# Kernel optimization log

Measured on AMD Instinct MI355X. Metric: run time of the kernel, lower is better.

The kernel has to match this reference:

```python
import jax, jax.numpy as jnp
import numpy as np

# dims
B, L, H, NH, D = 512, 200, 128, 4, 32      # batch, seq_len, hidden, heads (gnn & fcb), head dim H/NH
FT, TP, IP = 32, 64, 200                    # first_taxonomy_num, taxonomy/item nodes per graph
NHOP, NB = 2, 2                             # n_hop gnn layers, gip_block_nums
SH, FH = 512, 256                           # scb_hidden_units, fcb_hidden_units
ITEMS, TAX = 100001, 2000                   # item vocab (+pad row 0), taxonomy vocab
NT, NI = B * TP, B * IP                     # total taxonomy / item nodes in batched forest
DEG_I, DEG_T = 4, 2                         # in-degree per taxonomy node for i2t / t2t edges


def _ln(x, g, b, eps=1e-8):
    m = jnp.mean(x, -1, keepdims=True)
    v = jnp.mean((x - m) ** 2, -1, keepdims=True)
    return (x - m) / jnp.sqrt(v + eps) * g + b


def _gat(src_h, dst_h, es, ed, W, al, ar, bias):
    """DGL GATConv (eval mode): shared fc, leaky_relu(0.2) scores, segment softmax,
    identity residual (in == heads*out), bias, ReLU activation."""
    fs = (src_h @ W).reshape(-1, NH, D)                 # [Ns,NH,D]
    fd = (dst_h @ W).reshape(-1, NH, D)                 # [Nd,NH,D]
    el = jnp.sum(fs * al, -1)                           # [Ns,NH]
    er = jnp.sum(fd * ar, -1)                           # [Nd,NH]
    e = jax.nn.leaky_relu(el[es] + er[ed], 0.2)         # [E,NH]
    emax = jax.ops.segment_max(e, ed, num_segments=NT)
    a = jnp.exp(e - emax[ed])
    s = jax.ops.segment_sum(a, ed, num_segments=NT)
    alpha = a / s[ed]                                   # [E,NH]
    rst = jax.ops.segment_sum(alpha[..., None] * fs[es], ed, num_segments=NT)
    rst = rst + dst_h.reshape(-1, NH, D) + bias.reshape(NH, D)
    return jax.nn.relu(rst).reshape(-1, NH * D)


def _forward(item_embed, tax_embed, scb_ln_g, scb_ln_b, scb_w1, scb_w2, fcb_ln_g, fcb_ln_b,
             fcb_w1, fcb_w2, fcb_w3, wv, gi_w, gi_al, gi_ar, gi_b, gt_w, gt_al, gt_ar, gt_b,
             liw_g, liw_b, int_g, int_b, uni_w,
             seq, root, i2t_src, i2t_dst, t2t_src, t2t_dst, item_ids, tax_ids):
    # --- global intention: mixer-style blocks over the item sequence ---
    V = item_embed[seq]                                           # [B,L,H]
    for i in range(NB):
        nv = _ln(V, scb_ln_g[i], scb_ln_b[i])
        t = jax.nn.gelu(jnp.einsum('blh,ls->bhs', nv, scb_w1[i]), approximate=False)
        vs = nv + jnp.einsum('bhs,sl->blh', t, scb_w2[i])         # seq-mixing block
        nvs = _ln(vs, fcb_ln_g[i], fcb_ln_b[i])
        xh = nvs.reshape(B, L, NH, D)                             # fcb heads share w1/w2
        y = jax.nn.gelu(jnp.einsum('blkc,cf->blkf', xh, fcb_w1[i]), approximate=False)
        y = jnp.einsum('blkf,fc->blkc', y, fcb_w2[i]).reshape(B, L, H)
        V = nvs + y @ fcb_w3[i]
    alpha = jax.nn.softmax(V @ wv, axis=1)                        # [B,L]
    g = jnp.sum(alpha[..., None] * V, axis=1)                     # [B,H]
    # --- local intention: multi-hop hetero GAT on batched item-taxonomy forest ---
    item_h = item_embed[item_ids]                                 # [NI,H]
    tax_h = tax_embed[tax_ids]                                    # [NT,H]
    acc = jnp.zeros_like(tax_h)
    for hop in range(NHOP):
        t_i = _gat(item_h, tax_h, i2t_src, i2t_dst, gi_w[hop], gi_al[hop], gi_ar[hop], gi_b[hop])
        t_t = _gat(tax_h, tax_h, t2t_src, t2t_dst, gt_w[hop], gt_al[hop], gt_ar[hop], gt_b[hop])
        tax_h = t_i + t_t                                         # HeteroGraphConv 'sum'
        acc = acc + tax_h                                         # k_list accumulation
    total = acc / NHOP                                            # average over hops
    offs = jnp.arange(B) * TP                                     # batched-graph offsets (graph_taxonomy)
    valid = root != -1
    local = jnp.where(valid[..., None], total[jnp.clip(root, 0) + offs[:, None]], 0.0)  # [B,FT,H]
    # --- fuse global + local ---
    mul = jnp.einsum('bfh,bh->bf', local, g)                      # [B,FT]
    w = jax.nn.softmax(jnp.where(mul != 0, _ln(mul, liw_g, liw_b), -jnp.inf), axis=-1)
    intention = _ln(g + jnp.sum(w[..., None] * local, axis=1), int_g, int_b)
    return (intention @ uni_w) @ item_embed.T                     # [B, ITEMS]


def setup_inputs():
    key = jax.random.key(0)
    ks = jax.random.split(key, 32)
    nrm = lambda i, sh: jax.random.normal(ks[i], sh, jnp.float32) * 0.05
    inp = {}
    inp['seq'] = jax.random.randint(ks[0], (B, L), 0, ITEMS)
    inp['root'] = jax.random.randint(ks[1], (B, FT), 0, TP)       # all valid roots
    i2t_dst = jnp.repeat(jnp.arange(NT), DEG_I)
    inp['i2t_dst'] = i2t_dst
    inp['i2t_src'] = (i2t_dst // TP) * IP + jax.random.randint(ks[2], (NT * DEG_I,), 0, IP)
    t2t_dst = jnp.repeat(jnp.arange(NT), DEG_T)
    inp['t2t_dst'] = t2t_dst
    inp['t2t_src'] = (t2t_dst // TP) * TP + jax.random.randint(ks[3], (NT * DEG_T,), 0, TP)
    inp['item_ids'] = jax.random.randint(ks[4], (NI,), 1, ITEMS)
    inp['tax_ids'] = jax.random.randint(ks[5], (NT,), 1, TAX)
    inp['item_embed'] = nrm(6, (ITEMS, H)).at[0].set(0.0)         # padding_idx=0
    inp['tax_embed'] = nrm(7, (TAX, H)).at[0].set(0.0)
    inp['scb_ln_g'] = jnp.ones((NB, H)); inp['scb_ln_b'] = jnp.zeros((NB, H))
    inp['scb_w1'] = nrm(8, (NB, L, SH)); inp['scb_w2'] = nrm(9, (NB, SH, L))
    inp['fcb_ln_g'] = jnp.ones((NB, H)); inp['fcb_ln_b'] = jnp.zeros((NB, H))
    inp['fcb_w1'] = nrm(10, (NB, D, FH)); inp['fcb_w2'] = nrm(11, (NB, FH, D))
    inp['fcb_w3'] = nrm(12, (NB, H, H))
    inp['wv'] = nrm(13, (H,))
    inp['gi_w'] = nrm(14, (NHOP, H, H)); inp['gi_al'] = nrm(15, (NHOP, NH, D))
    inp['gi_ar'] = nrm(16, (NHOP, NH, D)); inp['gi_b'] = nrm(17, (NHOP, H))
    inp['gt_w'] = nrm(18, (NHOP, H, H)); inp['gt_al'] = nrm(19, (NHOP, NH, D))
    inp['gt_ar'] = nrm(20, (NHOP, NH, D)); inp['gt_b'] = nrm(21, (NHOP, H))
    inp['liw_g'] = jnp.ones((FT,)); inp['liw_b'] = jnp.zeros((FT,))
    inp['int_g'] = jnp.ones((H,)); inp['int_b'] = jnp.zeros((H,))
    inp['uni_w'] = nrm(22, (H, H))
    return inp


def reference(item_embed, tax_embed, scb_ln_g, scb_ln_b, scb_w1, scb_w2, fcb_ln_g, fcb_ln_b,
              fcb_w1, fcb_w2, fcb_w3, wv, gi_w, gi_al, gi_ar, gi_b, gt_w, gt_al, gt_ar, gt_b,
              liw_g, liw_b, int_g, int_b, uni_w,
              seq, root, i2t_src, i2t_dst, t2t_src, t2t_dst, item_ids, tax_ids):
    return _forward(item_embed, tax_embed, scb_ln_g, scb_ln_b, scb_w1, scb_w2, fcb_ln_g, fcb_ln_b,
                    fcb_w1, fcb_w2, fcb_w3, wv, gi_w, gi_al, gi_ar, gi_b, gt_w, gt_al, gt_ar, gt_b,
                    liw_g, liw_b, int_g, int_b, uni_w,
                    seq, root, i2t_src, i2t_dst, t2t_src, t2t_dst, item_ids, tax_ids)
```

## Files before the change

### kernel.cpp

```cpp
#include <hip/hip_runtime.h>
#include <hip/hip_bf16.h>

constexpr int TB = 512, TL = 200, TH = 128, TNH = 4, TD = 32;
constexpr int TFT = 32, TTP = 64, TIP = 200;
constexpr int TSH = 512, TFH = 256;
constexpr int TITEMS = 100001;
constexpr int TNT = TB * TTP;
constexpr int TNI = TB * TIP;
constexpr int TLP = 224;
constexpr int TIPAD = 100096;

typedef __attribute__((ext_vector_type(8))) short short8v;
typedef __attribute__((ext_vector_type(4))) float f32x4;

__device__ inline float gelu_fast(float x) {
    float u = x + 0.044715f * x * x * x;
    float e = exp2f(-2.302208f * u);
    return x / (1.0f + e);
}
__device__ inline unsigned short to_bf16u(float x) {
    __hip_bfloat16 h = __float2bfloat16(x);
    return *reinterpret_cast<unsigned short*>(&h);
}
__device__ inline float bfu_to_f(unsigned short u) {
    unsigned int x = ((unsigned int)u) << 16;
    return __uint_as_float(x);
}

__device__ inline float block_reduce_sum(float v, float* red) {
    for (int o = 32; o > 0; o >>= 1) v += __shfl_down(v, o, 64);
    int nw = blockDim.x >> 6;
    if ((threadIdx.x & 63) == 0) red[threadIdx.x >> 6] = v;
    __syncthreads();
    float r = 0.f;
    for (int w = 0; w < nw; ++w) r += red[w];
    __syncthreads();
    return r;
}

__global__ __launch_bounds__(256) void k_gather(const float* __restrict__ tab,
                                                const int* __restrict__ idx,
                                                float* __restrict__ out, int nrows) {
    int e = blockIdx.x * blockDim.x + threadIdx.x;
    if (e >= nrows * 32) return;
    int r = e >> 5, c = e & 31;
    ((float4*)out)[e] = ((const float4*)tab)[(size_t)idx[r] * 32 + c];
}

__global__ __launch_bounds__(256) void k_gather_bf(const float* __restrict__ tab,
                                                   const int* __restrict__ idx,
                                                   unsigned short* __restrict__ out, int nrows) {
    int e = blockIdx.x * blockDim.x + threadIdx.x;
    if (e >= nrows * 16) return;
    int r = e >> 4, c = e & 15;
    const float4 a = ((const float4*)tab)[(size_t)idx[r] * 32 + c * 2];
    const float4 b = ((const float4*)tab)[(size_t)idx[r] * 32 + c * 2 + 1];
    uint4 u;
    u.x = (unsigned int)to_bf16u(a.x) | ((unsigned int)to_bf16u(a.y) << 16);
    u.y = (unsigned int)to_bf16u(a.z) | ((unsigned int)to_bf16u(a.w) << 16);
    u.z = (unsigned int)to_bf16u(b.x) | ((unsigned int)to_bf16u(b.y) << 16);
    u.w = (unsigned int)to_bf16u(b.z) | ((unsigned int)to_bf16u(b.w) << 16);
    *(uint4*)(out + (size_t)e * 8) = u;
}

__global__ __launch_bounds__(256) void k_wcvt(const float* __restrict__ fw1, const float* __restrict__ fw2,
                                              const float* __restrict__ fw3, const float* __restrict__ giw,
                                              const float* __restrict__ gtw, unsigned short* __restrict__ WB) {
    int idx = blockIdx.x * 256 + threadIdx.x;
    float v;
    if (idx < 16384) {
        int nb = idx >> 13, r = idx & 8191, n = r >> 5, k = r & 31;
        v = fw1[(size_t)nb * 8192 + k * 256 + n];
    } else if (idx < 32768) {
        int t = idx - 16384;
        int nb = t >> 13, r = t & 8191, n = r >> 8, k = r & 255;
        v = fw2[(size_t)nb * 8192 + k * 32 + n];
    } else if (idx < 65536) {
        int t = idx - 32768;
        int nb = t >> 14, r = t & 16383, n = r >> 7, k = r & 127;
        v = fw3[(size_t)nb * 16384 + k * 128 + n];
    } else if (idx < 98304) {
        int t = idx - 65536;
        int hop = t >> 14, r = t & 16383, n = r >> 7, k = r & 127;
        v = giw[(size_t)hop * 16384 + k * 128 + n];
    } else {
        int t = idx - 98304;
        int hop = t >> 14, r = t & 16383, n = r >> 7, k = r & 127;
        v = gtw[(size_t)hop * 16384 + k * 128 + n];
    }
    WB[idx] = to_bf16u(v);
}

__global__ __launch_bounds__(128) void k_lnt(const float* __restrict__ V,
                                             const float* __restrict__ g, const float* __restrict__ b,
                                             float* __restrict__ NV, unsigned short* __restrict__ NVT) {
    __shared__ float tl[64][129];
    __shared__ float mrow[64], irow[64];
    int bb = blockIdx.y, l0 = blockIdx.x * 64, tid = threadIdx.x;
    for (int i = tid; i < 2048; i += 128) {
        int r = i >> 5, c = i & 31;
        int l = l0 + r;
        float4 v = {0.f, 0.f, 0.f, 0.f};
        if (l < TL) v = *(const float4*)(V + ((size_t)bb * TL + l) * TH + c * 4);
        tl[r][c * 4 + 0] = v.x; tl[r][c * 4 + 1] = v.y;
        tl[r][c * 4 + 2] = v.z; tl[r][c * 4 + 3] = v.w;
    }
    __syncthreads();
    {
        int row = tid >> 1, half = tid & 1;
        float s = 0.f, sq = 0.f;
        for (int k = 0; k < 64; ++k) {
            float v = tl[row][half * 64 + k];
            s += v; sq += v * v;
        }
        s += __shfl_xor(s, 1);
        sq += __shfl_xor(sq, 1);
        if (half == 0) {
            float mean = s * (1.f / 128.f);
            mrow[row] = mean;
            irow[row] = rsqrtf(sq * (1.f / 128.f) - mean * mean + 1e-8f);
        }
    }
    __syncthreads();
    for (int i = tid; i < 2048; i += 128) {
        int r = i >> 5, c = i & 31;
        int l = l0 + r;
        float4 o = {0.f, 0.f, 0.f, 0.f};
        if (l < TL) {
            float4 v = *(float4*)&tl[r][c * 4];
            float m = mrow[r], inv = irow[r];
            const float4 gg = ((const float4*)g)[c];
            const float4 bv = ((const float4*)b)[c];
            o.x = (v.x - m) * inv * gg.x + bv.x;
            o.y = (v.y - m) * inv * gg.y + bv.y;
            o.z = (v.z - m) * inv * gg.z + bv.z;
            o.w = (v.w - m) * inv * gg.w + bv.w;
            *(float4*)(NV + ((size_t)bb * TL + l) * TH + c * 4) = o;
        }
        *(float4*)&tl[r][c * 4] = o;
    }
    __syncthreads();
    int h = tid;
    int ng = (l0 + 64 > TLP) ? (TLP - l0) / 8 : 8;
    for (int lg = 0; lg < ng; ++lg) {
        uint4 u;
        unsigned int p[4];
#pragma unroll
        for (int q = 0; q < 4; ++q) {
            unsigned short ua = to_bf16u(tl[lg * 8 + q * 2 + 0][h]);
            unsigned short ub = to_bf16u(tl[lg * 8 + q * 2 + 1][h]);
            p[q] = (unsigned int)ua | ((unsigned int)ub << 16);
        }
        u.x = p[0]; u.y = p[1]; u.z = p[2]; u.w = p[3];
        *(uint4*)(NVT + ((size_t)bb * TH + h) * TLP + l0 + lg * 8) = u;
    }
}

__global__ __launch_bounds__(256) void k_wscb(const float* __restrict__ w1, const float* __restrict__ w2,
                                              unsigned short* __restrict__ W1T,
                                              unsigned short* __restrict__ W2T) {
    int bx = blockIdx.x;
    if (bx < TSH) {
        int s = bx, l = threadIdx.x;
        if (l < TLP) W1T[(size_t)s * TLP + l] = to_bf16u(l < TL ? w1[(size_t)l * TSH + s] : 0.f);
    } else {
        int l = bx - TSH;
        for (int it = 0; it < 2; ++it) {
            int s = it * 256 + threadIdx.x;
            W2T[(size_t)l * TSH + s] = to_bf16u(l < TL ? w2[(size_t)s * TL + l] : 0.f);
        }
    }
}

__global__ __launch_bounds__(256) void k_mm1(const unsigned short* __restrict__ NVT,
                                             const unsigned short* __restrict__ W1T,
                                             unsigned short* __restrict__ T, int bh) {
    __shared__ unsigned short As[128][40];
    __shared__ unsigned short Bs[128][40];
    int tid = threadIdx.x;
    int b_local = blockIdx.y, b = bh * 256 + b_local;
    int s0 = blockIdx.x * 128;
    int lane = tid & 63, wid = tid >> 6;
    int mw = wid >> 1, nw = wid & 1;
    f32x4 acc[4][4];
#pragma unroll
    for (int i = 0; i < 4; ++i)
#pragma unroll
        for (int j = 0; j < 4; ++j) acc[i][j] = (f32x4){0.f, 0.f, 0.f, 0.f};
    const unsigned short* Abase = NVT + (size_t)b * TH * TLP;
    const unsigned short* Bbase = W1T + (size_t)s0 * TLP;
    for (int kc = 0; kc < 7; ++kc) {
        __syncthreads();
        for (int i = tid; i < 512; i += 256) {
            int r = i >> 2, q = i & 3;
            *(uint4*)&As[r][q * 8] = *(const uint4*)(Abase + (size_t)r * TLP + kc * 32 + q * 8);
            *(uint4*)&Bs[r][q * 8] = *(const uint4*)(Bbase + (size_t)r * TLP + kc * 32 + q * 8);
        }
        __syncthreads();
        int ko = (lane >> 4) * 8;
        short8v af[4], bfr[4];
#pragma unroll
        for (int t = 0; t < 4; ++t) {
            af[t] = *(const short8v*)&As[mw * 64 + t * 16 + (lane & 15)][ko];
            bfr[t] = *(const short8v*)&Bs[nw * 64 + t * 16 + (lane & 15)][ko];
        }
#pragma unroll
        for (int i = 0; i < 4; ++i)
#pragma unroll
            for (int j = 0; j < 4; ++j)
                acc[i][j] = __builtin_amdgcn_mfma_f32_16x16x32_bf16(af[i], bfr[j], acc[i][j], 0, 0, 0);
    }
    int rbase = (lane >> 4) * 4, col = lane & 15;
#pragma unroll
    for (int i = 0; i < 4; ++i)
#pragma unroll
        for (int j = 0; j < 4; ++j) {
            int h0 = mw * 64 + i * 16 + rbase;
            int s = s0 + nw * 64 + j * 16 + col;
#pragma unroll
            for (int r = 0; r < 4; ++r)
                T[((size_t)b_local * TH + h0 + r) * TSH + s] = to_bf16u(gelu_fast(acc[i][j][r]));
        }
}

__global__ __launch_bounds__(256) void k_mm2l(const unsigned short* __restrict__ T,
                                              const unsigned short* __restrict__ W2T,
                                              float* __restrict__ NV,
                                              const float* __restrict__ lg, const float* __restrict__ lb,
                                              int bh) {
    __shared__ unsigned short As[128][40];
    __shared__ unsigned short Bs[64][40];
    __shared__ float vsl[64][132];
    __shared__ float mrow[64], irow[64];
    int tid = threadIdx.x;
    int b_local = blockIdx.y, b = bh * 256 + b_local;
    int l0 = blockIdx.x * 64;
    int lane = tid & 63, wid = tid >> 6;
    f32x4 acc[2][4];
#pragma unroll
    for (int i = 0; i < 2; ++i)
#pragma unroll
        for (int j = 0; j < 4; ++j) acc[i][j] = (f32x4){0.f, 0.f, 0.f, 0.f};
    const unsigned short* Abase = T + (size_t)b_local * TH * TSH;
    for (int kc = 0; kc < 16; ++kc) {
        __syncthreads();
        for (int i = tid; i < 512; i += 256) {
            int r = i >> 2, q = i & 3;
            *(uint4*)&As[r][q * 8] = *(const uint4*)(Abase + (size_t)r * TSH + kc * 32 + q * 8);
        }
        {
            int r = tid >> 2, q = tid & 3;
            int l = l0 + r;
            uint4 v = {0u, 0u, 0u, 0u};
            if (l < 208) v = *(const uint4*)(W2T + (size_t)l * TSH + kc * 32 + q * 8);
            *(uint4*)&Bs[r][q * 8] = v;
        }
        __syncthreads();
        int ko = (lane >> 4) * 8;
        short8v af[2], bfr[4];
#pragma unroll
        for (int t = 0; t < 2; ++t)
            af[t] = *(const short8v*)&As[wid * 32 + t * 16 + (lane & 15)][ko];
#pragma unroll
        for (int j = 0; j < 4; ++j)
            bfr[j] = *(const short8v*)&Bs[j * 16 + (lane & 15)][ko];
#pragma unroll
        for (int i = 0; i < 2; ++i)
#pragma unroll
            for (int j = 0; j < 4; ++j)
                acc[i][j] = __builtin_amdgcn_mfma_f32_16x16x32_bf16(af[i], bfr[j], acc[i][j], 0, 0, 0);
    }
    int rbase = (lane >> 4) * 4, col = lane & 15;
#pragma unroll
    for (int i = 0; i < 2; ++i)
#pragma unroll
        for (int j = 0; j < 4; ++j) {
            int l = l0 + j * 16 + col;
            int h0 = wid * 32 + i * 16 + rbase;
            float4 res = {0.f, 0.f, 0.f, 0.f};
            if (l < TL) res = *(const float4*)(NV + ((size_t)b * TL + l) * TH + h0);
            vsl[j * 16 + col][h0 + 0] = acc[i][j][0] + res.x;
            vsl[j * 16 + col][h0 + 1] = acc[i][j][1] + res.y;
            vsl[j * 16 + col][h0 + 2] = acc[i][j][2] + res.z;
            vsl[j * 16 + col][h0 + 3] = acc[i][j][3] + res.w;
        }
    __syncthreads();
    int row = tid >> 2, q = tid & 3;
    {
        float s = 0.f, sq = 0.f;
        for (int k = 0; k < 32; ++k) {
            float v = vsl[row][q * 32 + k];
            s += v; sq += v * v;
        }
        s += __shfl_xor(s, 1); s += __shfl_xor(s, 2);
        sq += __shfl_xor(sq, 1); sq += __shfl_xor(sq, 2);
        if (q == 0) {
            float mean = s * (1.f / 128.f);
            mrow[row] = mean;
            irow[row] = rsqrtf(sq * (1.f / 128.f) - mean * mean + 1e-8f);
        }
    }
    __syncthreads();
    {
        int l = l0 + row;
        if (l < TL) {
            float mean = mrow[row], inv = irow[row];
            float* dst = NV + ((size_t)b * TL + l) * TH + q * 32;
#pragma unroll
            for (int k4 = 0; k4 < 8; ++k4) {
                float4 v = *(float4*)&vsl[row][q * 32 + k4 * 4];
                const float4 gg = ((const float4*)lg)[q * 8 + k4];
                const float4 bv = ((const float4*)lb)[q * 8 + k4];
                float4 o;
                o.x = (v.x - mean) * inv * gg.x + bv.x;
                o.y = (v.y - mean) * inv * gg.y + bv.y;
                o.z = (v.z - mean) * inv * gg.z + bv.z;
                o.w = (v.w - mean) * inv * gg.w + bv.w;
                *(float4*)(dst + k4 * 4) = o;
            }
        }
    }
}

__global__ __launch_bounds__(256) void k_ffuse(const float* __restrict__ NV,
                                               const unsigned short* __restrict__ FW1B,
                                               const unsigned short* __restrict__ FW2B,
                                               unsigned short* __restrict__ Z) {
    __shared__ unsigned short As[64][40];
    __shared__ unsigned short BsBuf[256 * 40];
    __shared__ unsigned short Yl[64 * 264];
    int tid = threadIdx.x;
    int m0 = blockIdx.x * 64;
    int lane = tid & 63, wid = tid >> 6;
    for (int i = tid; i < 512; i += 256) {
        int r = i >> 3, q = i & 7;
        const float4 v = *(const float4*)(NV + (size_t)(m0 + r) * 32 + q * 4);
        ushort4 u;
        u.x = to_bf16u(v.x); u.y = to_bf16u(v.y); u.z = to_bf16u(v.z); u.w = to_bf16u(v.w);
        *(ushort4*)&As[r][q * 4] = u;
    }
    for (int i = tid; i < 1024; i += 256) {
        int r = i >> 2, q = i & 3;
        *(uint4*)&BsBuf[r * 40 + q * 8] = *(const uint4*)(FW1B + r * 32 + q * 8);
    }
    __syncthreads();
    int ko = (lane >> 4) * 8;
    short8v af[4], bfr[4];
#pragma unroll
    for (int t = 0; t < 4; ++t) {
        af[t] = *(const short8v*)&As[t * 16 + (lane & 15)][ko];
        bfr[t] = *(const short8v*)&BsBuf[(wid * 64 + t * 16 + (lane & 15)) * 40 + ko];
    }
    __syncthreads();
    {
        f32x4 acc[4][4];
#pragma unroll
        for (int i = 0; i < 4; ++i)
#pragma unroll
            for (int j = 0; j < 4; ++j) acc[i][j] = (f32x4){0.f, 0.f, 0.f, 0.f};
#pragma unroll
        for (int i = 0; i < 4; ++i)
#pragma unroll
            for (int j = 0; j < 4; ++j)
                acc[i][j] = __builtin_amdgcn_mfma_f32_16x16x32_bf16(af[i], bfr[j], acc[i][j], 0, 0, 0);
        int rbase = (lane >> 4) * 4, col = lane & 15;
#pragma unroll
        for (int i = 0; i < 4; ++i)
#pragma unroll
            for (int j = 0; j < 4; ++j)
#pragma unroll
                for (int r = 0; r < 4; ++r) {
                    int m = i * 16 + rbase + r;
                    int n = wid * 64 + j * 16 + col;
                    int idx = (m * 264 + n) ^ (((m >> 2) & 7) << 3);
                    Yl[idx] = to_bf16u(gelu_fast(acc[i][j][r]));
                }
    }
    for (int i = tid; i < 1024; i += 256) {
        int r = i >> 5, q = i & 31;
        *(uint4*)&BsBuf[r * 264 + q * 8] = *(const uint4*)(FW2B + r * 256 + q * 8);
    }
    __syncthreads();
    {
        f32x4 acc2[2];
        acc2[0] = (f32x4){0.f, 0.f, 0.f, 0.f};
        acc2[1] = (f32x4){0.f, 0.f, 0.f, 0.f};
        int mrow = wid * 16 + (lane & 15);
        int sw = ((mrow >> 2) & 7) << 3;
        for (int kc = 0; kc < 8; ++kc) {
            int ko2 = kc * 32 + (lane >> 4) * 8;
            short8v a2 = *(const short8v*)&Yl[(mrow * 264 + ko2) ^ sw];
            short8v b0 = *(const short8v*)&BsBuf[(lane & 15) * 264 + ko2];
            short8v b1 = *(const short8v*)&BsBuf[(16 + (lane & 15)) * 264 + ko2];
            acc2[0] = __builtin_amdgcn_mfma_f32_16x16x32_bf16(a2, b0, acc2[0], 0, 0, 0);
            acc2[1] = __builtin_amdgcn_mfma_f32_16x16x32_bf16(a2, b1, acc2[1], 0, 0, 0);
        }
        int rbase = (lane >> 4) * 4, col = lane & 15;
#pragma unroll
        for (int j = 0; j < 2; ++j)
#pragma unroll
            for (int r = 0; r < 4; ++r)
                Z[(size_t)(m0 + wid * 16 + rbase + r) * 32 + j * 16 + col] =
                    to_bf16u(acc2[j][r]);
    }
}

__global__ __launch_bounds__(256) void k_gmm_b(const unsigned short* __restrict__ A,
                                               const unsigned short* __restrict__ WB,
                                               const float* __restrict__ R,
                                               float* __restrict__ C) {
    __shared__ unsigned short As[128][40];
    __shared__ unsigned short Bs[128][40];
    int tid = threadIdx.x;
    int m0 = blockIdx.x * 128;
    int lane = tid & 63, wid = tid >> 6;
    int mw = wid >> 1, nw = wid & 1;
    f32x4 acc[4][4];
#pragma unroll
    for (int i = 0; i < 4; ++i)
#pragma unroll
        for (int j = 0; j < 4; ++j) acc[i][j] = (f32x4){0.f, 0.f, 0.f, 0.f};
    for (int kc = 0; kc < 4; ++kc) {
        __syncthreads();
        for (int i = tid; i < 512; i += 256) {
            int r = i >> 2, q = i & 3;
            *(uint4*)&As[r][q * 8] = *(const uint4*)(A + (size_t)(m0 + r) * TH + kc * 32 + q * 8);
            *(uint4*)&Bs[r][q * 8] = *(const uint4*)(WB + (size_t)r * TH + kc * 32 + q * 8);
        }
        __syncthreads();
        int ko = (lane >> 4) * 8;
        short8v af[4], bfr[4];
#pragma unroll
        for (int t = 0; t < 4; ++t) {
            af[t] = *(const short8v*)&As[mw * 64 + t * 16 + (lane & 15)][ko];
            bfr[t] = *(const short8v*)&Bs[nw * 64 + t * 16 + (lane & 15)][ko];
        }
#pragma unroll
        for (int i = 0; i < 4; ++i)
#pragma unroll
            for (int j = 0; j < 4; ++j)
                acc[i][j] = __builtin_amdgcn_mfma_f32_16x16x32_bf16(af[i], bfr[j], acc[i][j], 0, 0, 0);
    }
    int rbase = (lane >> 4) * 4, col = lane & 15;
#pragma unroll
    for (int i = 0; i < 4; ++i)
#pragma unroll
        for (int j = 0; j < 4; ++j) {
            int n = nw * 64 + j * 16 + col;
#pragma unroll
            for (int r = 0; r < 4; ++r) {
                size_t off = (size_t)(m0 + mw * 64 + i * 16 + rbase + r) * TH + n;
                float v = acc[i][j][r];
                if (R) v += R[off];
                C[off] = v;
            }
        }
}

__global__ __launch_bounds__(256) void k_gmm_bb(const unsigned short* __restrict__ A,
                                                const unsigned short* __restrict__ WB,
                                                unsigned short* __restrict__ C) {
    __shared__ unsigned short As[128][40];
    __shared__ unsigned short Bs[128][40];
    int tid = threadIdx.x;
    int m0 = blockIdx.x * 128;
    int lane = tid & 63, wid = tid >> 6;
    int mw = wid >> 1, nw = wid & 1;
    f32x4 acc[4][4];
#pragma unroll
    for (int i = 0; i < 4; ++i)
#pragma unroll
        for (int j = 0; j < 4; ++j) acc[i][j] = (f32x4){0.f, 0.f, 0.f, 0.f};
    for (int kc = 0; kc < 4; ++kc) {
        __syncthreads();
        for (int i = tid; i < 512; i += 256) {
            int r = i >> 2, q = i & 3;
            *(uint4*)&As[r][q * 8] = *(const uint4*)(A + (size_t)(m0 + r) * TH + kc * 32 + q * 8);
            *(uint4*)&Bs[r][q * 8] = *(const uint4*)(WB + (size_t)r * TH + kc * 32 + q * 8);
        }
        __syncthreads();
        int ko = (lane >> 4) * 8;
        short8v af[4], bfr[4];
#pragma unroll
        for (int t = 0; t < 4; ++t) {
            af[t] = *(const short8v*)&As[mw * 64 + t * 16 + (lane & 15)][ko];
            bfr[t] = *(const short8v*)&Bs[nw * 64 + t * 16 + (lane & 15)][ko];
        }
#pragma unroll
        for (int i = 0; i < 4; ++i)
#pragma unroll
            for (int j = 0; j < 4; ++j)
                acc[i][j] = __builtin_amdgcn_mfma_f32_16x16x32_bf16(af[i], bfr[j], acc[i][j], 0, 0, 0);
    }
    int rbase = (lane >> 4) * 4, col = lane & 15;
#pragma unroll
    for (int i = 0; i < 4; ++i)
#pragma unroll
        for (int j = 0; j < 4; ++j) {
            int n = nw * 64 + j * 16 + col;
#pragma unroll
            for (int r = 0; r < 4; ++r) {
                size_t off = (size_t)(m0 + mw * 64 + i * 16 + rbase + r) * TH + n;
                C[off] = to_bf16u(acc[i][j][r]);
            }
        }
}

__global__ __launch_bounds__(256) void k_pool(const float* __restrict__ V, const float* __restrict__ wv,
                                              float* __restrict__ g) {
    __shared__ float sc[TL];
    __shared__ float red[4];
    int b = blockIdx.x, tid = threadIdx.x;
    if (tid < TL) {
        float a = 0.f;
        const float* vp = V + (size_t)(b * TL + tid) * TH;
        for (int h = 0; h < TH; ++h) a += vp[h] * wv[h];
        sc[tid] = a;
    }
    __syncthreads();
    float m = (tid < TL) ? sc[tid] : -INFINITY;
    for (int o = 32; o > 0; o >>= 1) m = fmaxf(m, __shfl_down(m, o, 64));
    if ((tid & 63) == 0) red[tid >> 6] = m;
    __syncthreads();
    m = fmaxf(fmaxf(red[0], red[1]), fmaxf(red[2], red[3]));
    __syncthreads();
    float e = (tid < TL) ? expf(sc[tid] - m) : 0.f;
    float s = block_reduce_sum(e, red);
    if (tid < TL) sc[tid] = e / s;
    __syncthreads();
    if (tid < TH) {
        float a = 0.f;
        for (int l = 0; l < TL; ++l) a += sc[l] * V[(size_t)(b * TL + l) * TH + tid];
        g[b * TH + tid] = a;
    }
}

__global__ __launch_bounds__(256) void k_scores4(
        const unsigned short* __restrict__ f0, const float* __restrict__ v0, float* __restrict__ o0, int n0,
        const unsigned short* __restrict__ f1, const float* __restrict__ v1, float* __restrict__ o1, int n1,
        const unsigned short* __restrict__ f2, const float* __restrict__ v2, float* __restrict__ o2, int n2,
        const unsigned short* __restrict__ f3, const float* __restrict__ v3, float* __restrict__ o3, int n3) {
    int t = blockIdx.x * 256 + threadIdx.x;
    const unsigned short* f; const float* vec; float* o;
    if (t < n0 * 4) { f = f0; vec = v0; o = o0; }
    else {
        t -= n0 * 4;
        if (t < n1 * 4) { f = f1; vec = v1; o = o1; }
        else {
            t -= n1 * 4;
            if (t < n2 * 4) { f = f2; vec = v2; o = o2; }
            else {
                t -= n2 * 4;
                if (t >= n3 * 4) return;
                f = f3; vec = v3; o = o3;
            }
        }
    }
    int node = t >> 2, k = t & 3;
    const unsigned short* fp = f + (size_t)node * TH + k * TD;
    const float* vp = vec + k * TD;
    float a = 0.f;
#pragma unroll
    for (int q = 0; q < 4; ++q) {
        uint4 u = *(const uint4*)(fp + q * 8);
        unsigned int ws[4] = {u.x, u.y, u.z, u.w};
#pragma unroll
        for (int p = 0; p < 4; ++p) {
            a += __uint_as_float(ws[p] << 16) * vp[q * 8 + p * 2];
            a += __uint_as_float(ws[p] & 0xffff0000u) * vp[q * 8 + p * 2 + 1];
        }
    }
    o[t] = a;
}

__global__ __launch_bounds__(128) void k_gat(const unsigned short* __restrict__ tax_cur,
                                             const unsigned short* __restrict__ fs_i, const float* __restrict__ el_i,
                                             const float* __restrict__ er_i, const int* __restrict__ src_i,
                                             const float* __restrict__ bi,
                                             const unsigned short* __restrict__ fs_t, const float* __restrict__ el_t,
                                             const float* __restrict__ er_t, const int* __restrict__ src_t,
                                             const float* __restrict__ bt,
                                             unsigned short* __restrict__ tax_nxt,
                                             float* __restrict__ acc, int hop) {
    int n = blockIdx.x, h = threadIdx.x, k = h >> 5;
    float cur = bfu_to_f(tax_cur[(size_t)n * TH + h]);
    float ti, tt2;
    {
        float er = er_i[n * 4 + k];
        int s[4]; float e[4]; float m = -INFINITY;
#pragma unroll
        for (int j = 0; j < 4; ++j) {
            s[j] = src_i[n * 4 + j];
            float xx = el_i[s[j] * 4 + k] + er;
            e[j] = xx > 0.f ? xx : 0.2f * xx;
            m = fmaxf(m, e[j]);
        }
        float ssum = 0.f, av = 0.f;
#pragma unroll
        for (int j = 0; j < 4; ++j) {
            float a = expf(e[j] - m);
            ssum += a;
            av += a * bfu_to_f(fs_i[(size_t)s[j] * TH + h]);
        }
        ti = fmaxf(av / ssum + cur + bi[h], 0.f);
    }
    {
        float er = er_t[n * 4 + k];
        int s[2]; float e[2]; float m = -INFINITY;
#pragma unroll
        for (int j = 0; j < 2; ++j) {
            s[j] = src_t[n * 2 + j];
            float xx = el_t[s[j] * 4 + k] + er;
            e[j] = xx > 0.f ? xx : 0.2f * xx;
            m = fmaxf(m, e[j]);
        }
        float ssum = 0.f, av = 0.f;
#pragma unroll
        for (int j = 0; j < 2; ++j) {
            float a = expf(e[j] - m);
            ssum += a;
            av += a * bfu_to_f(fs_t[(size_t)s[j] * TH + h]);
        }
        tt2 = fmaxf(av / ssum + cur + bt[h], 0.f);
    }
    float nx = ti + tt2;
    size_t ai = (size_t)n * TH + h;
    tax_nxt[ai] = to_bf16u(nx);
    acc[ai] = (hop == 0) ? nx : acc[ai] + nx;
}

__global__ __launch_bounds__(128) void k_locfuse(const int* __restrict__ root, const float* __restrict__ acc,
                                                 const float* __restrict__ g,
                                                 const float* __restrict__ liw_g, const float* __restrict__ liw_b,
                                                 const float* __restrict__ int_g, const float* __restrict__ int_b,
                                                 const float* __restrict__ uni_w,
                                                 unsigned short* __restrict__ PB) {
    __shared__ float loc[TFT][TH];
    __shared__ float lm[TFT], wv_[TFT], inten[TH];
    __shared__ float red[2];
    int b = blockIdx.x, tid = threadIdx.x;
    float gv = g[b * TH + tid];
    for (int f = 0; f < TFT; ++f) {
        int r = root[b * TFT + f];
        float v = 0.f;
        if (r != -1) v = acc[(size_t)(b * TTP + (r < 0 ? 0 : r)) * TH + tid] * 0.5f;
        loc[f][tid] = v;
        float s = block_reduce_sum(v * gv, red);
        if (tid == 0) lm[f] = s;
    }
    __syncthreads();
    if (tid < TFT) {
        float mean = 0.f;
        for (int f = 0; f < TFT; ++f) mean += lm[f];
        mean *= (1.f / TFT);
        float var = 0.f;
        for (int f = 0; f < TFT; ++f) { float d = lm[f] - mean; var += d * d; }
        var *= (1.f / TFT);
        float ln = (lm[tid] - mean) * rsqrtf(var + 1e-8f) * liw_g[tid] + liw_b[tid];
        wv_[tid] = (lm[tid] != 0.f) ? ln : -INFINITY;
    }
    __syncthreads();
    if (tid < TFT) {
        float mx = -INFINITY;
        for (int f = 0; f < TFT; ++f) mx = fmaxf(mx, wv_[f]);
        float s = 0.f;
        for (int f = 0; f < TFT; ++f) s += expf(wv_[f] - mx);
        lm[tid] = expf(wv_[tid] - mx) / s;
    }
    __syncthreads();
    float ip = gv;
    for (int f = 0; f < TFT; ++f) ip += lm[f] * loc[f][tid];
    float mean = block_reduce_sum(ip, red) * (1.f / TH);
    float d = ip - mean;
    float var = block_reduce_sum(d * d, red) * (1.f / TH);
    inten[tid] = d * rsqrtf(var + 1e-8f) * int_g[tid] + int_b[tid];
    __syncthreads();
    float a = 0.f;
    for (int hp = 0; hp < TH; ++hp) a += inten[hp] * uni_w[hp * TH + tid];
    PB[(size_t)b * TH + tid] = to_bf16u(a);
}

__global__ __launch_bounds__(256) void k_ebc(const float* __restrict__ E,
                                             unsigned short* __restrict__ EB) {
    int t = blockIdx.x * 256 + threadIdx.x;
    if (t >= TIPAD * TH / 8) return;
    size_t base = (size_t)t * 8;
    int row = (int)(base >> 7);
    float4 a = {0.f, 0.f, 0.f, 0.f}, b = {0.f, 0.f, 0.f, 0.f};
    if (row < TITEMS) {
        a = *(const float4*)(E + base);
        b = *(const float4*)(E + base + 4);
    }
    ushort4 u0, u1;
    u0.x = to_bf16u(a.x); u0.y = to_bf16u(a.y); u0.z = to_bf16u(a.z); u0.w = to_bf16u(a.w);
    u1.x = to_bf16u(b.x); u1.y = to_bf16u(b.y); u1.z = to_bf16u(b.z); u1.w = to_bf16u(b.w);
    *(ushort4*)(EB + base) = u0;
    *(ushort4*)(EB + base + 4) = u1;
}

__global__ __launch_bounds__(256) void k_final_m(const unsigned short* __restrict__ PB,
                                                 const unsigned short* __restrict__ EB,
                                                 float* __restrict__ out) {
    __shared__ unsigned short Bs[128][136];
    int tid = threadIdx.x;
    int i0 = blockIdx.x * 128, b0 = blockIdx.y * 128;
    for (int i = tid; i < 2048; i += 256) {
        int r = i >> 4, q = i & 15;
        *(uint4*)&Bs[r][q * 8] = *(const uint4*)(EB + (size_t)(i0 + r) * TH + q * 8);
    }
    __syncthreads();
    int lane = tid & 63, wid = tid >> 6;
    int mw = wid >> 1, nw = wid & 1;
    f32x4 acc[4][4];
#pragma unroll
    for (int i = 0; i < 4; ++i)
#pragma unroll
        for (int j = 0; j < 4; ++j) acc[i][j] = (f32x4){0.f, 0.f, 0.f, 0.f};
#pragma unroll
    for (int kc = 0; kc < 4; ++kc) {
        int ko = kc * 32 + (lane >> 4) * 8;
        short8v af[4], bfr[4];
#pragma unroll
        for (int t = 0; t < 4; ++t) {
            af[t] = *(const short8v*)(PB + (size_t)(b0 + mw * 64 + t * 16 + (lane & 15)) * TH + ko);
            bfr[t] = *(const short8v*)&Bs[nw * 64 + t * 16 + (lane & 15)][ko];
        }
#pragma unroll
        for (int i = 0; i < 4; ++i)
#pragma unroll
            for (int j = 0; j < 4; ++j)
                acc[i][j] = __builtin_amdgcn_mfma_f32_16x16x32_bf16(af[i], bfr[j], acc[i][j], 0, 0, 0);
    }
    int rbase = (lane >> 4) * 4, col = lane & 15;
#pragma unroll
    for (int i = 0; i < 4; ++i)
#pragma unroll
        for (int j = 0; j < 4; ++j) {
            int ii = i0 + nw * 64 + j * 16 + col;
            if (ii < TITEMS) {
#pragma unroll
                for (int r = 0; r < 4; ++r)
                    out[(size_t)(b0 + mw * 64 + i * 16 + rbase + r) * TITEMS + ii] = acc[i][j][r];
            }
        }
}

extern "C" void kernel_launch(void* const* d_in, const int* in_sizes, int n_in,
                              void* d_out, int out_size, void* d_ws, size_t ws_size,
                              hipStream_t stream) {
    const int*   seq        = (const int*)d_in[0];
    const int*   root       = (const int*)d_in[1];
    const int*   i2t_src    = (const int*)d_in[3];
    const int*   t2t_src    = (const int*)d_in[5];
    const int*   item_ids   = (const int*)d_in[6];
    const int*   tax_ids    = (const int*)d_in[7];
    const float* item_embed = (const float*)d_in[8];
    const float* tax_embed  = (const float*)d_in[9];
    const float* scb_ln_g   = (const float*)d_in[10];
    const float* scb_ln_b   = (const float*)d_in[11];
    const float* scb_w1     = (const float*)d_in[12];
    const float* scb_w2     = (const float*)d_in[13];
    const float* fcb_ln_g   = (const float*)d_in[14];
    const float* fcb_ln_b   = (const float*)d_in[15];
    const float* fcb_w1     = (const float*)d_in[16];
    const float* fcb_w2     = (const float*)d_in[17];
    const float* fcb_w3     = (const float*)d_in[18];
    const float* wv         = (const float*)d_in[19];
    const float* gi_w       = (const float*)d_in[20];
    const float* gi_al      = (const float*)d_in[21];
    const float* gi_ar      = (const float*)d_in[22];
    const float* gi_b       = (const float*)d_in[23];
    const float* gt_w       = (const float*)d_in[24];
    const float* gt_al      = (const float*)d_in[25];
    const float* gt_ar      = (const float*)d_in[26];
    const float* gt_b       = (const float*)d_in[27];
    const float* liw_g      = (const float*)d_in[28];
    const float* liw_b      = (const float*)d_in[29];
    const float* int_g      = (const float*)d_in[30];
    const float* int_b      = (const float*)d_in[31];
    const float* uni_w      = (const float*)d_in[32];

    char* w = (char*)d_ws;
    float* V     = (float*)(w + 0);
    float* NV    = (float*)(w + 52428800);
    unsigned short* FSIB   = (unsigned short*)(w + 0);
    unsigned short* ITEMHB = (unsigned short*)(w + 52428800);
    unsigned short* NVT = (unsigned short*)(w + 104857600);
    unsigned short* T   = (unsigned short*)(w + 134217728);
    unsigned short* W1T = (unsigned short*)(w + 167772160);
    unsigned short* W2T = (unsigned short*)(w + 168001536);
    unsigned short* ZB  = (unsigned short*)(w + 104857600);
    unsigned short* TAXB0 = (unsigned short*)(w + 104857600);
    unsigned short* TAXB1 = (unsigned short*)(w + 113246208);
    float* ACC   = (float*)(w + 138412032);
    unsigned short* FDIB = (unsigned short*)(w + 155189248);
    unsigned short* FSTB = (unsigned short*)(w + 171966464);
    float* ELI   = (float*)(w + 188743680);
    float* ERI   = (float*)(w + 190382080);
    float* ELT   = (float*)(w + 190906368);
    float* ERT   = (float*)(w + 191430656);
    float* G     = (float*)(w + 200343552);
    unsigned short* WB = (unsigned short*)(w + 191954944);
    unsigned short* EB = (unsigned short*)(w + 155189248);
    unsigned short* PB = (unsigned short*)(w + 200671232);
    if (ws_size < 200933376ull) return;

    k_wcvt<<<512, 256, 0, stream>>>(fcb_w1, fcb_w2, fcb_w3, gi_w, gt_w, WB);

    k_gather<<<(TB * TL * 32 + 255) / 256, 256, 0, stream>>>(item_embed, seq, V, TB * TL);
    for (int nb = 0; nb < 2; ++nb) {
        k_lnt<<<dim3(4, TB), 128, 0, stream>>>(V, scb_ln_g + nb * TH, scb_ln_b + nb * TH, NV, NVT);
        k_wscb<<<720, 256, 0, stream>>>(scb_w1 + nb * TL * TSH, scb_w2 + nb * TSH * TL, W1T, W2T);
        for (int bh = 0; bh < 2; ++bh) {
            k_mm1<<<dim3(4, 256), 256, 0, stream>>>(NVT, W1T, T, bh);
            k_mm2l<<<dim3(4, 256), 256, 0, stream>>>(T, W2T, NV,
                                                     fcb_ln_g + nb * TH, fcb_ln_b + nb * TH, bh);
        }
        k_ffuse<<<TB * TL * 4 / 64, 256, 0, stream>>>(NV, WB + nb * 8192, WB + 16384 + nb * 8192, ZB);
        k_gmm_b<<<TB * TL / 128, 256, 0, stream>>>(ZB, WB + 32768 + nb * 16384, NV, V);
    }
    k_pool<<<TB, 256, 0, stream>>>(V, wv, G);

    k_gather_bf<<<(TNI * 16 + 255) / 256, 256, 0, stream>>>(item_embed, item_ids, ITEMHB, TNI);
    k_gather_bf<<<(TNT * 16 + 255) / 256, 256, 0, stream>>>(tax_embed, tax_ids, TAXB0, TNT);

    unsigned short* curb = TAXB0;
    unsigned short* nxtb = TAXB1;
    for (int hop = 0; hop < 2; ++hop) {
        const unsigned short* WiB = WB + 65536 + hop * 16384;
        const unsigned short* WtB = WB + 98304 + hop * 16384;
        k_gmm_bb<<<TNI / 128, 256, 0, stream>>>(ITEMHB, WiB, FSIB);
        k_gmm_bb<<<TNT / 128, 256, 0, stream>>>(curb, WiB, FDIB);
        k_gmm_bb<<<TNT / 128, 256, 0, stream>>>(curb, WtB, FSTB);
        int total = (TNI + 3 * TNT) * TNH;
        k_scores4<<<(total + 255) / 256, 256, 0, stream>>>(
            FSIB, gi_al + hop * TH, ELI, TNI,
            FDIB, gi_ar + hop * TH, ERI, TNT,
            FSTB, gt_al + hop * TH, ELT, TNT,
            FSTB, gt_ar + hop * TH, ERT, TNT);
        k_gat<<<TNT, 128, 0, stream>>>(curb, FSIB, ELI, ERI, i2t_src, gi_b + hop * TH,
                                       FSTB, ELT, ERT, t2t_src, gt_b + hop * TH, nxtb, ACC, hop);
        unsigned short* tmp = curb; curb = nxtb; nxtb = tmp;
    }

    k_locfuse<<<TB, 128, 0, stream>>>(root, ACC, G, liw_g, liw_b, int_g, int_b, uni_w, PB);
    k_ebc<<<(TIPAD * TH / 8 + 255) / 256, 256, 0, stream>>>(item_embed, EB);
    k_final_m<<<dim3(TIPAD / 128, TB / 128), 256, 0, stream>>>(PB, EB, (float*)d_out);
}
```

Before: 1.033 ms.

## Fuse sequence gather into layernorm, transpose MFMA outputs for packed stores, parallelize pool

```diff
diff --git a/kernel.cpp b/kernel.cpp
--- a/kernel.cpp
+++ b/kernel.cpp
@@ -36,15 +36,6 @@
     for (int w = 0; w < nw; ++w) r += red[w];
     __syncthreads();
     return r;
-}
-
-__global__ __launch_bounds__(256) void k_gather(const float* __restrict__ tab,
-                                                const int* __restrict__ idx,
-                                                float* __restrict__ out, int nrows) {
-    int e = blockIdx.x * blockDim.x + threadIdx.x;
-    if (e >= nrows * 32) return;
-    int r = e >> 5, c = e & 31;
-    ((float4*)out)[e] = ((const float4*)tab)[(size_t)idx[r] * 32 + c];
 }
 
 __global__ __launch_bounds__(256) void k_gather_bf(const float* __restrict__ tab,
@@ -92,6 +83,7 @@
 }
 
 __global__ __launch_bounds__(128) void k_lnt(const float* __restrict__ V,
+                                             const int* __restrict__ seqp, const float* __restrict__ tab,
                                              const float* __restrict__ g, const float* __restrict__ b,
                                              float* __restrict__ NV, unsigned short* __restrict__ NVT) {
     __shared__ float tl[64][129];
@@ -101,7 +93,11 @@
         int r = i >> 5, c = i & 31;
         int l = l0 + r;
         float4 v = {0.f, 0.f, 0.f, 0.f};
-        if (l < TL) v = *(const float4*)(V + ((size_t)bb * TL + l) * TH + c * 4);
+        if (l < TL) {
+            const float* src = seqp ? (tab + (size_t)seqp[bb * TL + l] * TH)
+                                    : (V + ((size_t)bb * TL + l) * TH);
+            v = *(const float4*)(src + c * 4);
+        }
         tl[r][c * 4 + 0] = v.x; tl[r][c * 4 + 1] = v.y;
         tl[r][c * 4 + 2] = v.z; tl[r][c * 4 + 3] = v.w;
     }
@@ -182,11 +178,11 @@
     int s0 = blockIdx.x * 128;
     int lane = tid & 63, wid = tid >> 6;
     int mw = wid >> 1, nw = wid & 1;
-    f32x4 acc[4][4];
-#pragma unroll
-    for (int i = 0; i < 4; ++i)
-#pragma unroll
-        for (int j = 0; j < 4; ++j) acc[i][j] = (f32x4){0.f, 0.f, 0.f, 0.f};
+    f32x4 accT[4][4];
+#pragma unroll
+    for (int j = 0; j < 4; ++j)
+#pragma unroll
+        for (int i = 0; i < 4; ++i) accT[j][i] = (f32x4){0.f, 0.f, 0.f, 0.f};
     const unsigned short* Abase = NVT + (size_t)b * TH * TLP;
     const unsigned short* Bbase = W1T + (size_t)s0 * TLP;
     for (int kc = 0; kc < 7; ++kc) {
@@ -205,21 +201,24 @@
             bfr[t] = *(const short8v*)&Bs[nw * 64 + t * 16 + (lane & 15)][ko];
         }
 #pragma unroll
-        for (int i = 0; i < 4; ++i)
-#pragma unroll
-            for (int j = 0; j < 4; ++j)
-                acc[i][j] = __builtin_amdgcn_mfma_f32_16x16x32_bf16(af[i], bfr[j], acc[i][j], 0, 0, 0);
+        for (int j = 0; j < 4; ++j)
+#pragma unroll
+            for (int i = 0; i < 4; ++i)
+                accT[j][i] = __builtin_amdgcn_mfma_f32_16x16x32_bf16(bfr[j], af[i], accT[j][i], 0, 0, 0);
     }
     int rbase = (lane >> 4) * 4, col = lane & 15;
 #pragma unroll
     for (int i = 0; i < 4; ++i)
 #pragma unroll
         for (int j = 0; j < 4; ++j) {
-            int h0 = mw * 64 + i * 16 + rbase;
-            int s = s0 + nw * 64 + j * 16 + col;
-#pragma unroll
-            for (int r = 0; r < 4; ++r)
-                T[((size_t)b_local * TH + h0 + r) * TSH + s] = to_bf16u(gelu_fast(acc[i][j][r]));
+            int h = mw * 64 + i * 16 + col;
+            int sb = s0 + nw * 64 + j * 16 + rbase;
+            ushort4 pk;
+            pk.x = to_bf16u(gelu_fast(accT[j][i][0]));
+            pk.y = to_bf16u(gelu_fast(accT[j][i][1]));
+            pk.z = to_bf16u(gelu_fast(accT[j][i][2]));
+            pk.w = to_bf16u(gelu_fast(accT[j][i][3]));
+            *(ushort4*)(T + ((size_t)b_local * TH + h) * TSH + sb) = pk;
         }
 }
 
@@ -279,10 +278,12 @@
             int h0 = wid * 32 + i * 16 + rbase;
             float4 res = {0.f, 0.f, 0.f, 0.f};
             if (l < TL) res = *(const float4*)(NV + ((size_t)b * TL + l) * TH + h0);
-            vsl[j * 16 + col][h0 + 0] = acc[i][j][0] + res.x;
-            vsl[j * 16 + col][h0 + 1] = acc[i][j][1] + res.y;
-            vsl[j * 16 + col][h0 + 2] = acc[i][j][2] + res.z;
-            vsl[j * 16 + col][h0 + 3] = acc[i][j][3] + res.w;
+            float4 o;
+            o.x = acc[i][j][0] + res.x;
+            o.y = acc[i][j][1] + res.y;
+            o.z = acc[i][j][2] + res.z;
+            o.w = acc[i][j][3] + res.w;
+            *(float4*)&vsl[j * 16 + col][h0] = o;
         }
     __syncthreads();
     int row = tid >> 2, q = tid & 3;
@@ -332,6 +333,7 @@
     int tid = threadIdx.x;
     int m0 = blockIdx.x * 64;
     int lane = tid & 63, wid = tid >> 6;
+    int col = lane & 15, rbase = (lane >> 4) * 4, ko = (lane >> 4) * 8;
     for (int i = tid; i < 512; i += 256) {
         int r = i >> 3, q = i & 7;
         const float4 v = *(const float4*)(NV + (size_t)(m0 + r) * 32 + q * 4);
@@ -344,37 +346,38 @@
         *(uint4*)&BsBuf[r * 40 + q * 8] = *(const uint4*)(FW1B + r * 32 + q * 8);
     }
     __syncthreads();
-    int ko = (lane >> 4) * 8;
     short8v af[4], bfr[4];
 #pragma unroll
     for (int t = 0; t < 4; ++t) {
-        af[t] = *(const short8v*)&As[t * 16 + (lane & 15)][ko];
-        bfr[t] = *(const short8v*)&BsBuf[(wid * 64 + t * 16 + (lane & 15)) * 40 + ko];
+        af[t] = *(const short8v*)&As[t * 16 + col][ko];
+        bfr[t] = *(const short8v*)&BsBuf[(wid * 64 + t * 16 + col) * 40 + ko];
     }
     __syncthreads();
     {
-        f32x4 acc[4][4];
+        f32x4 yt[4][4];
+#pragma unroll
+        for (int j = 0; j < 4; ++j)
+#pragma unroll
+            for (int i = 0; i < 4; ++i) yt[j][i] = (f32x4){0.f, 0.f, 0.f, 0.f};
+#pragma unroll
+        for (int j = 0; j < 4; ++j)
+#pragma unroll
+            for (int i = 0; i < 4; ++i)
+                yt[j][i] = __builtin_amdgcn_mfma_f32_16x16x32_bf16(bfr[j], af[i], yt[j][i], 0, 0, 0);
 #pragma unroll
         for (int i = 0; i < 4; ++i)
 #pragma unroll
-            for (int j = 0; j < 4; ++j) acc[i][j] = (f32x4){0.f, 0.f, 0.f, 0.f};
-#pragma unroll
-        for (int i = 0; i < 4; ++i)
-#pragma unroll
-            for (int j = 0; j < 4; ++j)
-                acc[i][j] = __builtin_amdgcn_mfma_f32_16x16x32_bf16(af[i], bfr[j], acc[i][j], 0, 0, 0);
-        int rbase = (lane >> 4) * 4, col = lane & 15;
-#pragma unroll
-        for (int i = 0; i < 4; ++i)
-#pragma unroll
-            for (int j = 0; j < 4; ++j)
-#pragma unroll
-                for (int r = 0; r < 4; ++r) {
-                    int m = i * 16 + rbase + r;
-                    int n = wid * 64 + j * 16 + col;
-                    int idx = (m * 264 + n) ^ (((m >> 2) & 7) << 3);
-                    Yl[idx] = to_bf16u(gelu_fast(acc[i][j][r]));
-                }
+            for (int j = 0; j < 4; ++j) {
+                int m = i * 16 + col;
+                int n0 = wid * 64 + j * 16 + rbase;
+                ushort4 pk;
+                pk.x = to_bf16u(gelu_fast(yt[j][i][0]));
+                pk.y = to_bf16u(gelu_fast(yt[j][i][1]));
+                pk.z = to_bf16u(gelu_fast(yt[j][i][2]));
+                pk.w = to_bf16u(gelu_fast(yt[j][i][3]));
+                int idx = (m * 264 + n0) ^ (((m >> 2) & 7) << 3);
+                *(ushort4*)&Yl[idx] = pk;
+            }
     }
     for (int i = tid; i < 1024; i += 256) {
         int r = i >> 5, q = i & 31;
@@ -385,17 +388,16 @@
         f32x4 acc2[2];
         acc2[0] = (f32x4){0.f, 0.f, 0.f, 0.f};
         acc2[1] = (f32x4){0.f, 0.f, 0.f, 0.f};
-        int mrow = wid * 16 + (lane & 15);
+        int mrow = wid * 16 + col;
         int sw = ((mrow >> 2) & 7) << 3;
         for (int kc = 0; kc < 8; ++kc) {
-            int ko2 = kc * 32 + (lane >> 4) * 8;
+            int ko2 = kc * 32 + ko;
             short8v a2 = *(const short8v*)&Yl[(mrow * 264 + ko2) ^ sw];
-            short8v b0 = *(const short8v*)&BsBuf[(lane & 15) * 264 + ko2];
-            short8v b1 = *(const short8v*)&BsBuf[(16 + (lane & 15)) * 264 + ko2];
+            short8v b0 = *(const short8v*)&BsBuf[col * 264 + ko2];
+            short8v b1 = *(const short8v*)&BsBuf[(16 + col) * 264 + ko2];
             acc2[0] = __builtin_amdgcn_mfma_f32_16x16x32_bf16(a2, b0, acc2[0], 0, 0, 0);
             acc2[1] = __builtin_amdgcn_mfma_f32_16x16x32_bf16(a2, b1, acc2[1], 0, 0, 0);
         }
-        int rbase = (lane >> 4) * 4, col = lane & 15;
 #pragma unroll
         for (int j = 0; j < 2; ++j)
 #pragma unroll
@@ -466,11 +468,11 @@
     int m0 = blockIdx.x * 128;
     int lane = tid & 63, wid = tid >> 6;
     int mw = wid >> 1, nw = wid & 1;
-    f32x4 acc[4][4];
-#pragma unroll
-    for (int i = 0; i < 4; ++i)
-#pragma unroll
-        for (int j = 0; j < 4; ++j) acc[i][j] = (f32x4){0.f, 0.f, 0.f, 0.f};
+    f32x4 accT[4][4];
+#pragma unroll
+    for (int j = 0; j < 4; ++j)
+#pragma unroll
+        for (int i = 0; i < 4; ++i) accT[j][i] = (f32x4){0.f, 0.f, 0.f, 0.f};
     for (int kc = 0; kc < 4; ++kc) {
         __syncthreads();
         for (int i = tid; i < 512; i += 256) {
@@ -487,22 +489,24 @@
             bfr[t] = *(const short8v*)&Bs[nw * 64 + t * 16 + (lane & 15)][ko];
         }
 #pragma unroll
-        for (int i = 0; i < 4; ++i)
-#pragma unroll
-            for (int j = 0; j < 4; ++j)
-                acc[i][j] = __builtin_amdgcn_mfma_f32_16x16x32_bf16(af[i], bfr[j], acc[i][j], 0, 0, 0);
+        for (int j = 0; j < 4; ++j)
+#pragma unroll
+            for (int i = 0; i < 4; ++i)
+                accT[j][i] = __builtin_amdgcn_mfma_f32_16x16x32_bf16(bfr[j], af[i], accT[j][i], 0, 0, 0);
     }
     int rbase = (lane >> 4) * 4, col = lane & 15;
 #pragma unroll
     for (int i = 0; i < 4; ++i)
 #pragma unroll
         for (int j = 0; j < 4; ++j) {
-            int n = nw * 64 + j * 16 + col;
-#pragma unroll
-            for (int r = 0; r < 4; ++r) {
-                size_t off = (size_t)(m0 + mw * 64 + i * 16 + rbase + r) * TH + n;
-                C[off] = to_bf16u(acc[i][j][r]);
-            }
+            int m = m0 + mw * 64 + i * 16 + col;
+            int n0 = nw * 64 + j * 16 + rbase;
+            ushort4 pk;
+            pk.x = to_bf16u(accT[j][i][0]);
+            pk.y = to_bf16u(accT[j][i][1]);
+            pk.z = to_bf16u(accT[j][i][2]);
+            pk.w = to_bf16u(accT[j][i][3]);
+            *(ushort4*)(C + (size_t)m * TH + n0) = pk;
         }
 }
 
@@ -511,11 +515,12 @@
     __shared__ float sc[TL];
     __shared__ float red[4];
     int b = blockIdx.x, tid = threadIdx.x;
-    if (tid < TL) {
-        float a = 0.f;
-        const float* vp = V + (size_t)(b * TL + tid) * TH;
-        for (int h = 0; h < TH; ++h) a += vp[h] * wv[h];
-        sc[tid] = a;
+    int lane = tid & 63, w = tid >> 6;
+    for (int l = w; l < TL; l += 4) {
+        const float2 v = ((const float2*)(V + (size_t)(b * TL + l) * TH))[lane];
+        float a = v.x * wv[2 * lane] + v.y * wv[2 * lane + 1];
+        for (int o = 32; o > 0; o >>= 1) a += __shfl_down(a, o, 64);
+        if (lane == 0) sc[l] = a;
     }
     __syncthreads();
     float m = (tid < TL) ? sc[tid] : -INFINITY;
@@ -807,9 +812,9 @@
 
     k_wcvt<<<512, 256, 0, stream>>>(fcb_w1, fcb_w2, fcb_w3, gi_w, gt_w, WB);
 
-    k_gather<<<(TB * TL * 32 + 255) / 256, 256, 0, stream>>>(item_embed, seq, V, TB * TL);
     for (int nb = 0; nb < 2; ++nb) {
-        k_lnt<<<dim3(4, TB), 128, 0, stream>>>(V, scb_ln_g + nb * TH, scb_ln_b + nb * TH, NV, NVT);
+        k_lnt<<<dim3(4, TB), 128, 0, stream>>>(V, nb == 0 ? seq : nullptr, item_embed,
+                                               scb_ln_g + nb * TH, scb_ln_b + nb * TH, NV, NVT);
         k_wscb<<<720, 256, 0, stream>>>(scb_w1 + nb * TL * TSH, scb_w2 + nb * TSH * TL, W1T, W2T);
         for (int bh = 0; bh < 2; ++bh) {
             k_mm1<<<dim3(4, 256), 256, 0, stream>>>(NVT, W1T, T, bh);
```

Result: no change. 1.028 ms (-0.5%).
